# Optimization experiments

Measured on AMD Instinct MI355X. Metric: run time of the kernel, lower is better.

The kernel has to match this reference:

```python
import jax, jax.numpy as jnp
import numpy as np

N, E, H = 50000, 800000, 128

def _lin_params(key, out_dim, in_dim, bias=True, gain=1.0):
    k1, k2 = jax.random.split(key)
    lim = gain * np.sqrt(6.0 / (in_dim + out_dim))
    W = jax.random.uniform(k1, (out_dim, in_dim), jnp.float32, -lim, lim)
    b = jax.random.uniform(k2, (out_dim,), jnp.float32, -lim, lim) if bias else None
    return W, b

def setup_inputs() -> dict:
    key = jax.random.key(0)
    ks = jax.random.split(key, 12)
    h = jax.random.normal(ks[0], (N, H), jnp.float32)
    x = jax.random.normal(ks[1], (N, 3), jnp.float32)
    edge_index = jax.random.randint(ks[2], (2, E), 0, N, jnp.int64)
    We1, be1 = _lin_params(ks[3], H, 2 * H + 1)
    We2, be2 = _lin_params(ks[4], H, H)
    Wn1, bn1 = _lin_params(ks[5], H, 2 * H)
    Wn2, bn2 = _lin_params(ks[6], H, H)
    Wc1, bc1 = _lin_params(ks[7], H, H)
    Wc2, _ = _lin_params(ks[8], 1, H, bias=False, gain=0.001)
    gamma = jnp.ones((H,), jnp.float32)
    beta = jnp.zeros((H,), jnp.float32)
    return {"h": h, "x": x, "edge_index": edge_index,
            "We1": We1, "be1": be1, "We2": We2, "be2": be2,
            "Wn1": Wn1, "bn1": bn1, "Wn2": Wn2, "bn2": bn2,
            "Wc1": Wc1, "bc1": bc1, "Wc2": Wc2,
            "gamma": gamma, "beta": beta}

def _layer_norm(y, gamma, beta, eps=1e-5):
    mu = jnp.mean(y, axis=-1, keepdims=True)
    var = jnp.var(y, axis=-1, keepdims=True)
    return (y - mu) * jax.lax.rsqrt(var + eps) * gamma + beta

def reference(h, x, edge_index, We1, be1, We2, be2, Wn1, bn1, Wn2, bn2,
              Wc1, bc1, Wc2, gamma, beta):
    src, dst = edge_index[0], edge_index[1]
    diff = x[src] - x[dst]                                  # (E, 3)
    dist_sq = jnp.sum(diff * diff, axis=-1, keepdims=True)  # (E, 1)
    edge_in = jnp.concatenate([h[src], h[dst], dist_sq], axis=-1)  # (E, 2H+1)
    m = jax.nn.silu(edge_in @ We1.T + be1)
    m = jax.nn.silu(m @ We2.T + be2)                        # (E, H)
    num_nodes = h.shape[0]
    agg = jax.ops.segment_sum(m, dst, num_segments=num_nodes)            # (N, H)
    count = jax.ops.segment_sum(jnp.ones((dst.shape[0], 1), h.dtype), dst,
                                num_segments=num_nodes)
    count = jnp.maximum(count, 1.0)
    agg = agg / count
    u = jax.nn.silu(jnp.concatenate([h, agg], axis=-1) @ Wn1.T + bn1)
    h_out = h + (u @ Wn2.T + bn2)
    h_out = _layer_norm(h_out, gamma, beta)
    cw = jax.nn.silu(m @ Wc1.T + bc1) @ Wc2.T               # (E, 1)
    coord_agg = jax.ops.segment_sum(diff * cw, dst, num_segments=num_nodes) / count
    x_out = x + coord_agg
    return h_out, x_out
```

## Files before the change

kernel.cpp:

```cpp
#include <hip/hip_runtime.h>
#include <stdint.h>

using bf16x8 = __attribute__((ext_vector_type(8))) short;
using f32x4  = __attribute__((ext_vector_type(4))) float;

__device__ __forceinline__ unsigned short f2bf(float f) {
  uint32_t x = __float_as_uint(f);
  x += 0x7fffu + ((x >> 16) & 1u);
  return (unsigned short)(x >> 16);
}
__device__ __forceinline__ float bf2f(unsigned short u) {
  return __uint_as_float(((uint32_t)u) << 16);
}
__device__ __forceinline__ uint32_t cvtpk2(float lo, float hi) {
  uint32_t r;
  asm("v_cvt_pk_bf16_f32 %0, %1, %2" : "=v"(r) : "v"(lo), "v"(hi));
  return r;
}
__device__ __forceinline__ float silu_f(float v) {
  float e = __expf(-v);
  return v * __builtin_amdgcn_rcpf(1.0f + e);
}
__device__ __forceinline__ void unpack2(uint32_t u, float& lo, float& hi) {
  lo = __uint_as_float(u << 16);
  hi = __uint_as_float(u & 0xffff0000u);
}

__device__ __forceinline__ int msoff(int row, int col) {
  return row * 136 + ((((col >> 3) + row * 4) & 15) << 3) + (col & 7);
}
__device__ __forceinline__ int msoff_slot(int row, int slot) {
  return row * 136 + (((slot + row * 4) & 15) << 3);
}

__global__ void prep_kernel(const float* __restrict__ We1, const float* __restrict__ We2,
                            const float* __restrict__ Wn1, const float* __restrict__ Wn2,
                            const float* __restrict__ Wc1, const int* __restrict__ ei,
                            unsigned short* __restrict__ W1p, unsigned short* __restrict__ W2b,
                            unsigned short* __restrict__ N1b, unsigned short* __restrict__ N2b,
                            unsigned short* __restrict__ W3b, float* __restrict__ w1c,
                            int* __restrict__ flag) {
  int i = blockIdx.x * 256 + threadIdx.x;
  if (i < 256 * 128) {
    int c = i >> 7, k = i & 127;
    W1p[i] = f2bf(We1[(size_t)(c & 127) * 257 + ((c >> 7) << 7) + k]);
    N1b[i] = f2bf(Wn1[i]);
  }
  if (i < 128 * 128) {
    W2b[i] = f2bf(We2[i]);
    W3b[i] = f2bf(Wc1[i]);
    N2b[i] = f2bf(Wn2[i]);
  }
  if (i < 128) w1c[i] = We1[i * 257 + 256];
  if (i == 0) {
    int allz = 1;
    for (int k = 0; k < 64; ++k) allz &= (ei[2 * k + 1] == 0);
    *flag = allz;
  }
}

__global__ void hist_kernel(const int* __restrict__ ei, const int* __restrict__ flag,
                            int* __restrict__ deg, int E) {
  int e = blockIdx.x * 256 + threadIdx.x;
  if (e >= E) return;
  int d = (*flag) ? (int)((const long long*)ei)[(size_t)E + e] : ei[E + e];
  atomicAdd(&deg[d], 1);
}

__global__ void scanA_kernel(const int* __restrict__ deg, int* __restrict__ offs,
                             int* __restrict__ bsum, int N) {
  __shared__ int sh[256];
  int t = threadIdx.x, idx = blockIdx.x * 256 + t;
  int v = (idx < N) ? deg[idx] : 0;
  sh[t] = v;
  __syncthreads();
#pragma unroll
  for (int d = 1; d < 256; d <<= 1) {
    int u = (t >= d) ? sh[t - d] : 0;
    __syncthreads();
    sh[t] += u;
    __syncthreads();
  }
  if (idx < N) offs[idx] = sh[t] - v;
  if (t == 255) bsum[blockIdx.x] = sh[255];
}

__global__ void scanB_kernel(int* __restrict__ bsum, int* __restrict__ offs,
                             int nb, int N) {
  __shared__ int sh[256];
  int t = threadIdx.x;
  int v = (t < nb) ? bsum[t] : 0;
  sh[t] = v;
  __syncthreads();
#pragma unroll
  for (int d = 1; d < 256; d <<= 1) {
    int u = (t >= d) ? sh[t - d] : 0;
    __syncthreads();
    sh[t] += u;
    __syncthreads();
  }
  bsum[t] = sh[t] - v;
  if (t == 255) offs[N] = sh[255];
}

__global__ void scanC_kernel(const int* __restrict__ bsum, int* __restrict__ offs,
                             int* __restrict__ cursor, int N) {
  int idx = blockIdx.x * 256 + threadIdx.x;
  if (idx < N) {
    int o = offs[idx] + bsum[blockIdx.x];
    offs[idx] = o;
    cursor[idx] = o;
  }
}

__global__ void scatter_kernel(const int* __restrict__ ei, const int* __restrict__ flag,
                               int* __restrict__ cursor, int2* __restrict__ sd_s, int E) {
  int e = blockIdx.x * 256 + threadIdx.x;
  if (e >= E) return;
  int s, d;
  if (*flag) {
    s = (int)((const long long*)ei)[e];
    d = (int)((const long long*)ei)[(size_t)E + e];
  } else {
    s = ei[e];
    d = ei[E + e];
  }
  int pos = atomicAdd(&cursor[d], 1);
  int2 p; p.x = s; p.y = d;
  sd_s[pos] = p;
}

__global__ __launch_bounds__(256) void proj_kernel(
    const float* __restrict__ h, const float* __restrict__ be1,
    const unsigned short* __restrict__ W1p,
    unsigned short* __restrict__ Ps, unsigned short* __restrict__ Pd, int N) {
  const int tid = threadIdx.x;
  const int base = blockIdx.x * 64;
  const int w = tid >> 6, lane = tid & 63, lg = lane >> 4, lr = lane & 15;

  f32x4 acc[4][4];
#pragma unroll
  for (int m = 0; m < 4; ++m)
#pragma unroll
    for (int n = 0; n < 4; ++n) { f32x4 z = {0.f,0.f,0.f,0.f}; acc[m][n] = z; }

#pragma unroll
  for (int k0 = 0; k0 < 4; ++k0) {
    bf16x8 b[4];
#pragma unroll
    for (int n = 0; n < 4; ++n)
      b[n] = *(const bf16x8*)(W1p + ((w * 64 + n * 16 + lr) << 7) + k0 * 32 + lg * 8);
#pragma unroll
    for (int m = 0; m < 4; ++m) {
      int row = base + m * 16 + lr; if (row >= N) row = N - 1;
      const float* p = h + (size_t)row * 128 + k0 * 32 + lg * 8;
      float4 fa = *(const float4*)p;
      float4 fb = *(const float4*)(p + 4);
      uint32_t u0 = cvtpk2(fa.x, fa.y), u1 = cvtpk2(fa.z, fa.w);
      uint32_t u2 = cvtpk2(fb.x, fb.y), u3 = cvtpk2(fb.z, fb.w);
      union { uint32_t u[4]; bf16x8 v; } cv;
      cv.u[0] = u0; cv.u[1] = u1; cv.u[2] = u2; cv.u[3] = u3;
#pragma unroll
      for (int n = 0; n < 4; ++n)
        acc[m][n] = __builtin_amdgcn_mfma_f32_16x16x32_bf16(cv.v, b[n], acc[m][n], 0, 0, 0);
    }
  }
#pragma unroll
  for (int n = 0; n < 4; ++n) {
    int o = w * 64 + n * 16 + lr;
    unsigned short* dstp = (o < 128) ? Ps : Pd;
    int oo = o & 127;
    float add = (o < 128) ? be1[o] : 0.f;
#pragma unroll
    for (int m = 0; m < 4; ++m)
#pragma unroll
      for (int r = 0; r < 4; ++r) {
        int row = base + m * 16 + lg * 4 + r;
        if (row < N) dstp[(size_t)row * 128 + oo] = f2bf(acc[m][n][r] + add);
      }
  }
}

__global__ __launch_bounds__(256, 6) void edge_kernel(
    const unsigned short* __restrict__ Ps, const unsigned short* __restrict__ Pd,
    const float* __restrict__ x, const int2* __restrict__ sd_s,
    const float* __restrict__ w1c,
    const float* __restrict__ be2, const float* __restrict__ bc1,
    const float* __restrict__ Wc2,
    const unsigned short* __restrict__ W2b, const unsigned short* __restrict__ W3b,
    float* __restrict__ aggH, float* __restrict__ coordX, int E) {
  __shared__ __align__(16) unsigned short Ms[64 * 136];
  __shared__ float swred[4][64];
  __shared__ int   ssrc[64], sdst[64];
  __shared__ float sds[64];
  __shared__ float sdif[64][3];

  const int tid   = threadIdx.x;
  const int tbase = blockIdx.x * 64;
  const int w = tid >> 6, lane = tid & 63, lg = lane >> 4, lr = lane & 15;

  if (tid < 64) {
    int pos = tbase + tid;
    int s = 0, d = 0;
    if (pos < E) { int2 p = sd_s[pos]; s = p.x; d = p.y; }
    ssrc[tid] = s; sdst[tid] = d;
    float dx = x[s * 3 + 0] - x[d * 3 + 0];
    float dy = x[s * 3 + 1] - x[d * 3 + 1];
    float dz = x[s * 3 + 2] - x[d * 3 + 2];
    sdif[tid][0] = dx; sdif[tid][1] = dy; sdif[tid][2] = dz;
    sds[tid] = dx * dx + dy * dy + dz * dz;
  }
  __syncthreads();

  {
    const float4* w4 = (const float4*)w1c;
#pragma unroll
    for (int ch = 0; ch < 2; ++ch) {
      uint4 av[2], bv[2];
#pragma unroll
      for (int it = 0; it < 2; ++it) {
        int idx = tid + (ch * 2 + it) * 256;
        int e = idx >> 4, seg = idx & 15;
        av[it] = *(const uint4*)(Ps + (size_t)ssrc[e] * 128 + seg * 8);
        bv[it] = *(const uint4*)(Pd + (size_t)sdst[e] * 128 + seg * 8);
      }
#pragma unroll
      for (int it = 0; it < 2; ++it) {
        int idx = tid + (ch * 2 + it) * 256;
        int e = idx >> 4, seg = idx & 15;
        float dsv = sds[e];
        float4 wA = w4[seg * 2], wB = w4[seg * 2 + 1];
        float a0,a1,a2,a3,a4,a5,a6,a7, b0,b1,b2,b3,b4,b5,b6,b7;
        unpack2(((uint32_t*)&av[it])[0], a0, a1);
        unpack2(((uint32_t*)&av[it])[1], a2, a3);
        unpack2(((uint32_t*)&av[it])[2], a4, a5);
        unpack2(((uint32_t*)&av[it])[3], a6, a7);
        unpack2(((uint32_t*)&bv[it])[0], b0, b1);
        unpack2(((uint32_t*)&bv[it])[1], b2, b3);
        unpack2(((uint32_t*)&bv[it])[2], b4, b5);
        unpack2(((uint32_t*)&bv[it])[3], b6, b7);
        float v0 = silu_f(a0 + b0 + dsv * wA.x);
        float v1 = silu_f(a1 + b1 + dsv * wA.y);
        float v2 = silu_f(a2 + b2 + dsv * wA.z);
        float v3 = silu_f(a3 + b3 + dsv * wA.w);
        float v4 = silu_f(a4 + b4 + dsv * wB.x);
        float v5 = silu_f(a5 + b5 + dsv * wB.y);
        float v6 = silu_f(a6 + b6 + dsv * wB.z);
        float v7 = silu_f(a7 + b7 + dsv * wB.w);
        uint4 o;
        o.x = cvtpk2(v0, v1); o.y = cvtpk2(v2, v3);
        o.z = cvtpk2(v4, v5); o.w = cvtpk2(v6, v7);
        *(uint4*)(&Ms[msoff_slot(e, seg)]) = o;
      }
    }
  }
  __syncthreads();

  {
    f32x4 acc[4][2];
#pragma unroll
    for (int m = 0; m < 4; ++m) { f32x4 z = {0.f,0.f,0.f,0.f}; acc[m][0] = z; acc[m][1] = z; }
#pragma unroll
    for (int k0 = 0; k0 < 4; ++k0) {
      bf16x8 b0 = *(const bf16x8*)(W2b + ((w * 32 + lr)      << 7) + k0 * 32 + lg * 8);
      bf16x8 b1 = *(const bf16x8*)(W2b + ((w * 32 + 16 + lr) << 7) + k0 * 32 + lg * 8);
#pragma unroll
      for (int m = 0; m < 4; ++m) {
        int row = m * 16 + lr;
        bf16x8 a = *(const bf16x8*)(&Ms[msoff_slot(row, k0 * 4 + lg)]);
        acc[m][0] = __builtin_amdgcn_mfma_f32_16x16x32_bf16(a, b0, acc[m][0], 0, 0, 0);
        acc[m][1] = __builtin_amdgcn_mfma_f32_16x16x32_bf16(a, b1, acc[m][1], 0, 0, 0);
      }
    }
    uint32_t pk[4][2][2];
#pragma unroll
    for (int n = 0; n < 2; ++n) {
      int o = w * 32 + n * 16 + lr;
      float b2v = be2[o];
#pragma unroll
      for (int m = 0; m < 4; ++m)
#pragma unroll
        for (int r = 0; r < 4; r += 2)
          pk[m][n][r >> 1] = cvtpk2(silu_f(acc[m][n][r] + b2v),
                                    silu_f(acc[m][n][r + 1] + b2v));
    }
    __syncthreads();
#pragma unroll
    for (int n = 0; n < 2; ++n) {
      int o = w * 32 + n * 16 + lr;
#pragma unroll
      for (int m = 0; m < 4; ++m)
#pragma unroll
        for (int r = 0; r < 4; r += 2) {
          int row = m * 16 + lg * 4 + r;
          uint32_t u = pk[m][n][r >> 1];
          Ms[msoff(row, o)]     = (unsigned short)(u & 0xffffu);
          Ms[msoff(row + 1, o)] = (unsigned short)(u >> 16);
        }
    }
  }
  __syncthreads();

  {
    f32x4 acc[4][2];
#pragma unroll
    for (int m = 0; m < 4; ++m) { f32x4 z = {0.f,0.f,0.f,0.f}; acc[m][0] = z; acc[m][1] = z; }
#pragma unroll
    for (int k0 = 0; k0 < 4; ++k0) {
      bf16x8 b0 = *(const bf16x8*)(W3b + ((w * 32 + lr)      << 7) + k0 * 32 + lg * 8);
      bf16x8 b1 = *(const bf16x8*)(W3b + ((w * 32 + 16 + lr) << 7) + k0 * 32 + lg * 8);
#pragma unroll
      for (int m = 0; m < 4; ++m) {
        int row = m * 16 + lr;
        bf16x8 a = *(const bf16x8*)(&Ms[msoff_slot(row, k0 * 4 + lg)]);
        acc[m][0] = __builtin_amdgcn_mfma_f32_16x16x32_bf16(a, b0, acc[m][0], 0, 0, 0);
        acc[m][1] = __builtin_amdgcn_mfma_f32_16x16x32_bf16(a, b1, acc[m][1], 0, 0, 0);
      }
    }
    float pr[4][4];
#pragma unroll
    for (int m = 0; m < 4; ++m)
#pragma unroll
      for (int r = 0; r < 4; ++r) pr[m][r] = 0.f;
#pragma unroll
    for (int n = 0; n < 2; ++n) {
      int o = w * 32 + n * 16 + lr;
      float b3 = bc1[o], wc = Wc2[o];
#pragma unroll
      for (int m = 0; m < 4; ++m)
#pragma unroll
        for (int r = 0; r < 4; ++r)
          pr[m][r] += silu_f(acc[m][n][r] + b3) * wc;
    }
#pragma unroll
    for (int m = 0; m < 4; ++m)
#pragma unroll
      for (int r = 0; r < 4; ++r) {
        float v = pr[m][r];
        v += __shfl_xor(v, 1); v += __shfl_xor(v, 2);
        v += __shfl_xor(v, 4); v += __shfl_xor(v, 8);
        pr[m][r] = v;
      }
    if (lr == 0) {
#pragma unroll
      for (int m = 0; m < 4; ++m)
#pragma unroll
        for (int r = 0; r < 4; ++r)
          swred[w][m * 16 + lg * 4 + r] = pr[m][r];
    }
  }
  __syncthreads();

  const int nv = min(64, E - tbase);
  if (tid < 128) {
    int cp = tid & 63, hf = tid >> 6;
    int c0 = cp * 2;
    int e0 = hf * 32;
    int nvh = min(32, nv - e0);
    if (nvh > 0) {
      float r0 = 0.f, r1 = 0.f;
      int prev = sdst[e0];
#pragma unroll 4
      for (int j = 0; j < nvh; ++j) {
        int e = e0 + j;
        int d = sdst[e];
        uint32_t u = *(const uint32_t*)(&Ms[msoff(e, c0)]);
        if (d != prev) {
          atomicAdd(&aggH[(size_t)prev * 128 + c0],     r0);
          atomicAdd(&aggH[(size_t)prev * 128 + c0 + 1], r1);
          r0 = 0.f; r1 = 0.f; prev = d;
        }
        float lo, hi; unpack2(u, lo, hi);
        r0 += lo; r1 += hi;
      }
      atomicAdd(&aggH[(size_t)prev * 128 + c0],     r0);
      atomicAdd(&aggH[(size_t)prev * 128 + c0 + 1], r1);
    }
  } else if (tid >= 192 && tid < 198) {
    int t6 = tid - 192;
    int c3 = t6 % 3, hf = t6 / 3;
    int e0 = hf * 32;
    int nvh = min(32, nv - e0);
    if (nvh > 0) {
      float run = 0.f;
      int prev = sdst[e0];
#pragma unroll 4
      for (int j = 0; j < nvh; ++j) {
        int e = e0 + j;
        int d = sdst[e];
        float cwv = swred[0][e] + swred[1][e] + swred[2][e] + swred[3][e];
        if (d != prev) {
          atomicAdd(&coordX[(size_t)prev * 3 + c3], run);
          run = 0.f; prev = d;
        }
        run += sdif[e][c3] * cwv;
      }
      atomicAdd(&coordX[(size_t)prev * 3 + c3], run);
    }
  }
}

__global__ __launch_bounds__(256) void node_kernel(
    const float* __restrict__ h, const float* __restrict__ x,
    const float* __restrict__ bn1, const float* __restrict__ bn2,
    const float* __restrict__ gamma, const float* __restrict__ beta,
    const unsigned short* __restrict__ N1b, const unsigned short* __restrict__ N2b,
    float* __restrict__ aggH, float* __restrict__ coordX,
    const int* __restrict__ deg, int N) {
  __shared__ __align__(16) unsigned short In[64][264];
  __shared__ __align__(16) unsigned short U[64][136];
  __shared__ float scnt[64];

  const int tid  = threadIdx.x;
  const int base = blockIdx.x * 64;
  const int w    = tid >> 6;
  const int lane = tid & 63;
  const int lg   = lane >> 4, lr = lane & 15;
  const int w16  = w * 16;

  if (tid < 64) {
    int n = base + tid;
    scnt[tid] = (n < N) ? fmaxf((float)deg[n], 1.0f) : 1.0f;
  }
  __syncthreads();

#pragma unroll
  for (int it = 0; it < 8; ++it) {
    int idx = tid + it * 256;
    int i = idx >> 5, seg = idx & 31;
    int n = base + i; if (n >= N) n = N - 1;
    float sc = 1.0f;
    const float* p;
    if (seg < 16) { p = h + (size_t)n * 128 + seg * 8; }
    else          { p = aggH + (size_t)n * 128 + (seg - 16) * 8; sc = 1.0f / scnt[i]; }
    float4 a = *(const float4*)p;
    float4 b = *(const float4*)(p + 4);
    uint32_t u0 = cvtpk2(a.x * sc, a.y * sc);
    uint32_t u1 = cvtpk2(a.z * sc, a.w * sc);
    uint32_t u2 = cvtpk2(b.x * sc, b.y * sc);
    uint32_t u3 = cvtpk2(b.z * sc, b.w * sc);
    uint4 v = {u0, u1, u2, u3};
    *(uint4*)&In[i][seg * 8] = v;
  }
  __syncthreads();

  {
    f32x4 acc[8];
#pragma unroll
    for (int n = 0; n < 8; ++n) { f32x4 z = {0.f,0.f,0.f,0.f}; acc[n] = z; }
#pragma unroll
    for (int k0 = 0; k0 < 8; ++k0) {
      bf16x8 a = *(const bf16x8*)(&In[w16 + lr][k0 * 32 + lg * 8]);
#pragma unroll
      for (int n = 0; n < 8; ++n) {
        bf16x8 b = *(const bf16x8*)(N1b + ((n * 16 + lr) << 8) + k0 * 32 + lg * 8);
        acc[n] = __builtin_amdgcn_mfma_f32_16x16x32_bf16(a, b, acc[n], 0, 0, 0);
      }
    }
#pragma unroll
    for (int n = 0; n < 8; ++n) {
      int o = n * 16 + lr;
      float b1 = bn1[o];
#pragma unroll
      for (int r = 0; r < 4; ++r) {
        int me = lg * 4 + r;
        U[w16 + me][o] = f2bf(silu_f(acc[n][r] + b1));
      }
    }
  }

  float* hp = (float*)&In[0][0];
  {
    f32x4 acc[8];
#pragma unroll
    for (int n = 0; n < 8; ++n) { f32x4 z = {0.f,0.f,0.f,0.f}; acc[n] = z; }
#pragma unroll
    for (int k0 = 0; k0 < 4; ++k0) {
      bf16x8 a = *(const bf16x8*)(&U[w16 + lr][k0 * 32 + lg * 8]);
#pragma unroll
      for (int n = 0; n < 8; ++n) {
        bf16x8 b = *(const bf16x8*)(N2b + ((n * 16 + lr) << 7) + k0 * 32 + lg * 8);
        acc[n] = __builtin_amdgcn_mfma_f32_16x16x32_bf16(a, b, acc[n], 0, 0, 0);
      }
    }
#pragma unroll
    for (int n = 0; n < 8; ++n) {
      int o = n * 16 + lr;
      float b2 = bn2[o];
#pragma unroll
      for (int r = 0; r < 4; ++r) {
        int me = w16 + lg * 4 + r;
        int ng = base + me; if (ng >= N) ng = N - 1;
        hp[(size_t)me * 132 + o] = acc[n][r] + b2 + h[(size_t)ng * 128 + o];
      }
    }
  }
  __syncthreads();

  {
    int r = tid >> 2, q = tid & 3;
    int ng = base + r;
    float s = 0.f, s2 = 0.f;
#pragma unroll
    for (int j = 0; j < 32; ++j) {
      float v = hp[(size_t)r * 132 + j * 4 + q];
      s += v; s2 += v * v;
    }
    s  += __shfl_xor(s, 1);  s  += __shfl_xor(s, 2);
    s2 += __shfl_xor(s2, 1); s2 += __shfl_xor(s2, 2);
    float mu  = s * (1.0f / 128.0f);
    float var = s2 * (1.0f / 128.0f) - mu * mu;
    float rs  = rsqrtf(var + 1e-5f);
    if (ng < N) {
#pragma unroll
      for (int j = 0; j < 32; ++j) {
        int o = j * 4 + q;
        float v = (hp[(size_t)r * 132 + o] - mu) * rs * gamma[o] + beta[o];
        aggH[(size_t)ng * 128 + o] = v;
      }
    }
  }

  if (tid < 192) {
    int i = tid / 3, c = tid % 3;
    int n2 = base + i;
    if (n2 < N) {
      size_t off = (size_t)n2 * 3 + c;
      coordX[off] = x[off] + coordX[off] / scnt[i];
    }
  }
}

extern "C" void kernel_launch(void* const* d_in, const int* in_sizes, int n_in,
                              void* d_out, int out_size, void* d_ws, size_t ws_size,
                              hipStream_t stream) {
  const float* h    = (const float*)d_in[0];
  const float* x    = (const float*)d_in[1];
  const int*   ei   = (const int*)d_in[2];
  const float* We1  = (const float*)d_in[3];
  const float* be1  = (const float*)d_in[4];
  const float* We2  = (const float*)d_in[5];
  const float* be2  = (const float*)d_in[6];
  const float* Wn1  = (const float*)d_in[7];
  const float* bn1  = (const float*)d_in[8];
  const float* Wn2  = (const float*)d_in[9];
  const float* bn2  = (const float*)d_in[10];
  const float* Wc1  = (const float*)d_in[11];
  const float* bc1  = (const float*)d_in[12];
  const float* Wc2  = (const float*)d_in[13];
  const float* gamma = (const float*)d_in[14];
  const float* beta  = (const float*)d_in[15];

  int N = in_sizes[0] / 128;
  int E = in_sizes[2] / 2;

  float* aggH   = (float*)d_out;
  float* coordX = (float*)d_out + (size_t)N * 128;

  char* ws = (char*)d_ws;
  size_t off = 0;
  auto alloc = [&](size_t bytes) {
    char* p = ws + off;
    off = (off + bytes + 255) & ~(size_t)255;
    return p;
  };
  unsigned short* Ps     = (unsigned short*)alloc((size_t)N * 128 * 2);
  unsigned short* Pd     = (unsigned short*)alloc((size_t)N * 128 * 2);
  unsigned short* W1p    = (unsigned short*)alloc(256 * 128 * 2);
  unsigned short* W2b    = (unsigned short*)alloc(128 * 128 * 2);
  unsigned short* N1b    = (unsigned short*)alloc(128 * 256 * 2);
  unsigned short* N2b    = (unsigned short*)alloc(128 * 128 * 2);
  unsigned short* W3b    = (unsigned short*)alloc(128 * 128 * 2);
  float*          w1c    = (float*)alloc(128 * 4);
  int*            flag   = (int*)alloc(4);
  int*            deg    = (int*)alloc((size_t)N * 4);
  int*            offs   = (int*)alloc(((size_t)N + 1) * 4);
  int*            cursor = (int*)alloc((size_t)N * 4);
  int*            bsum   = (int*)alloc(256 * 4);
  int2*           sd_s   = (int2*)alloc((size_t)E * 8);
  (void)ws_size;

  int nb = (N + 255) / 256;

  hipMemsetAsync(d_out, 0, (size_t)out_size * 4, stream);
  hipMemsetAsync(deg, 0, (size_t)N * 4, stream);

  prep_kernel<<<128, 256, 0, stream>>>(We1, We2, Wn1, Wn2, Wc1, ei,
                                       W1p, W2b, N1b, N2b, W3b, w1c, flag);
  hist_kernel<<<(E + 255) / 256, 256, 0, stream>>>(ei, flag, deg, E);
  scanA_kernel<<<nb, 256, 0, stream>>>(deg, offs, bsum, N);
  scanB_kernel<<<1, 256, 0, stream>>>(bsum, offs, nb, N);
  scanC_kernel<<<nb, 256, 0, stream>>>(bsum, offs, cursor, N);
  scatter_kernel<<<(E + 255) / 256, 256, 0, stream>>>(ei, flag, cursor, sd_s, E);
  proj_kernel<<<(N + 63) / 64, 256, 0, stream>>>(h, be1, W1p, Ps, Pd, N);
  edge_kernel<<<(E + 63) / 64, 256, 0, stream>>>(Ps, Pd, x, sd_s, w1c,
                                                 be2, bc1, Wc2, W2b, W3b,
                                                 aggH, coordX, E);
  node_kernel<<<(N + 63) / 64, 256, 0, stream>>>(h, x, bn1, bn2, gamma, beta, N1b, N2b,
                                                 aggH, coordX, deg, N);
}
```

Before: 379.3 us.

## Remap edge blocks per XCD, widen scatter threads, and stream node inputs directly

The edge kernel now remaps block IDs so consecutive logical edge tiles land on the same XCD, which keeps L2 locality for the sorted-by-destination atomics. The scatter phase now uses all 256 threads, each covering 16 edges instead of 32, and the coordinate scatter uses 12 threads. The node kernel drops the staging LDS buffer and loads h/agg rows straight from global memory into MFMA A operands, sharing one buffer for U and hp. This cuts shared memory to raise occupancy, at the cost of more atomics and repeated global loads across k0.

After: 393.6 us. +3.8%, slower.

```diff
diff --git a/kernel.cpp b/kernel.cpp
--- a/kernel.cpp
+++ b/kernel.cpp
@@ -196,13 +196,17 @@
   __shared__ float sdif[64][3];
 
   const int tid   = threadIdx.x;
-  const int tbase = blockIdx.x * 64;
+  const int nwg = gridDim.x;
+  const int q = nwg >> 3, r = nwg & 7;
+  const int xcd = blockIdx.x & 7, pos = blockIdx.x >> 3;
+  const int logical = (xcd < r ? xcd * (q + 1) : r * (q + 1) + (xcd - r) * q) + pos;
+  const int tbase = logical * 64;
   const int w = tid >> 6, lane = tid & 63, lg = lane >> 4, lr = lane & 15;
 
   if (tid < 64) {
-    int pos = tbase + tid;
+    int p0 = tbase + tid;
     int s = 0, d = 0;
-    if (pos < E) { int2 p = sd_s[pos]; s = p.x; d = p.y; }
+    if (p0 < E) { int2 p = sd_s[p0]; s = p.x; d = p.y; }
     ssrc[tid] = s; sdst[tid] = d;
     float dx = x[s * 3 + 0] - x[d * 3 + 0];
     float dy = x[s * 3 + 1] - x[d * 3 + 1];
@@ -280,9 +284,9 @@
 #pragma unroll
       for (int m = 0; m < 4; ++m)
 #pragma unroll
-        for (int r = 0; r < 4; r += 2)
-          pk[m][n][r >> 1] = cvtpk2(silu_f(acc[m][n][r] + b2v),
-                                    silu_f(acc[m][n][r + 1] + b2v));
+        for (int r2 = 0; r2 < 4; r2 += 2)
+          pk[m][n][r2 >> 1] = cvtpk2(silu_f(acc[m][n][r2] + b2v),
+                                     silu_f(acc[m][n][r2 + 1] + b2v));
     }
     __syncthreads();
 #pragma unroll
@@ -291,9 +295,9 @@
 #pragma unroll
       for (int m = 0; m < 4; ++m)
 #pragma unroll
-        for (int r = 0; r < 4; r += 2) {
-          int row = m * 16 + lg * 4 + r;
-          uint32_t u = pk[m][n][r >> 1];
+        for (int r2 = 0; r2 < 4; r2 += 2) {
+          int row = m * 16 + lg * 4 + r2;
+          uint32_t u = pk[m][n][r2 >> 1];
           Ms[msoff(row, o)]     = (unsigned short)(u & 0xffffu);
           Ms[msoff(row + 1, o)] = (unsigned short)(u >> 16);
         }
@@ -321,7 +325,7 @@
 #pragma unroll
     for (int m = 0; m < 4; ++m)
 #pragma unroll
-      for (int r = 0; r < 4; ++r) pr[m][r] = 0.f;
+      for (int r2 = 0; r2 < 4; ++r2) pr[m][r2] = 0.f;
 #pragma unroll
     for (int n = 0; n < 2; ++n) {
       int o = w * 32 + n * 16 + lr;
@@ -329,34 +333,34 @@
 #pragma unroll
       for (int m = 0; m < 4; ++m)
 #pragma unroll
-        for (int r = 0; r < 4; ++r)
-          pr[m][r] += silu_f(acc[m][n][r] + b3) * wc;
+        for (int r2 = 0; r2 < 4; ++r2)
+          pr[m][r2] += silu_f(acc[m][n][r2] + b3) * wc;
     }
 #pragma unroll
     for (int m = 0; m < 4; ++m)
 #pragma unroll
-      for (int r = 0; r < 4; ++r) {
-        float v = pr[m][r];
+      for (int r2 = 0; r2 < 4; ++r2) {
+        float v = pr[m][r2];
         v += __shfl_xor(v, 1); v += __shfl_xor(v, 2);
         v += __shfl_xor(v, 4); v += __shfl_xor(v, 8);
-        pr[m][r] = v;
+        pr[m][r2] = v;
       }
     if (lr == 0) {
 #pragma unroll
       for (int m = 0; m < 4; ++m)
 #pragma unroll
-        for (int r = 0; r < 4; ++r)
-          swred[w][m * 16 + lg * 4 + r] = pr[m][r];
+        for (int r2 = 0; r2 < 4; ++r2)
+          swred[w][m * 16 + lg * 4 + r2] = pr[m][r2];
     }
   }
   __syncthreads();
 
   const int nv = min(64, E - tbase);
-  if (tid < 128) {
-    int cp = tid & 63, hf = tid >> 6;
+  {
+    int cp = tid & 63, qt = tid >> 6;
     int c0 = cp * 2;
-    int e0 = hf * 32;
-    int nvh = min(32, nv - e0);
+    int e0 = qt * 16;
+    int nvh = min(16, nv - e0);
     if (nvh > 0) {
       float r0 = 0.f, r1 = 0.f;
       int prev = sdst[e0];
@@ -376,11 +380,11 @@
       atomicAdd(&aggH[(size_t)prev * 128 + c0],     r0);
       atomicAdd(&aggH[(size_t)prev * 128 + c0 + 1], r1);
     }
-  } else if (tid >= 192 && tid < 198) {
-    int t6 = tid - 192;
-    int c3 = t6 % 3, hf = t6 / 3;
-    int e0 = hf * 32;
-    int nvh = min(32, nv - e0);
+  }
+  if (tid < 12) {
+    int c3 = tid % 3, qt = tid / 3;
+    int e0 = qt * 16;
+    int nvh = min(16, nv - e0);
     if (nvh > 0) {
       float run = 0.f;
       int prev = sdst[e0];
@@ -407,9 +411,9 @@
     const unsigned short* __restrict__ N1b, const unsigned short* __restrict__ N2b,
     float* __restrict__ aggH, float* __restrict__ coordX,
     const int* __restrict__ deg, int N) {
-  __shared__ __align__(16) unsigned short In[64][264];
-  __shared__ __align__(16) unsigned short U[64][136];
+  __shared__ __align__(16) float hp[64 * 132];
   __shared__ float scnt[64];
+  unsigned short* U = (unsigned short*)hp;
 
   const int tid  = threadIdx.x;
   const int base = blockIdx.x * 64;
@@ -424,25 +428,8 @@
   }
   __syncthreads();
 
-#pragma unroll
-  for (int it = 0; it < 8; ++it) {
-    int idx = tid + it * 256;
-    int i = idx >> 5, seg = idx & 31;
-    int n = base + i; if (n >= N) n = N - 1;
-    float sc = 1.0f;
-    const float* p;
-    if (seg < 16) { p = h + (size_t)n * 128 + seg * 8; }
-    else          { p = aggH + (size_t)n * 128 + (seg - 16) * 8; sc = 1.0f / scnt[i]; }
-    float4 a = *(const float4*)p;
-    float4 b = *(const float4*)(p + 4);
-    uint32_t u0 = cvtpk2(a.x * sc, a.y * sc);
-    uint32_t u1 = cvtpk2(a.z * sc, a.w * sc);
-    uint32_t u2 = cvtpk2(b.x * sc, b.y * sc);
-    uint32_t u3 = cvtpk2(b.z * sc, b.w * sc);
-    uint4 v = {u0, u1, u2, u3};
-    *(uint4*)&In[i][seg * 8] = v;
-  }
-  __syncthreads();
+  int arow = base + w16 + lr; if (arow >= N) arow = N - 1;
+  const float sc = 1.0f / scnt[w16 + lr];
 
   {
     f32x4 acc[8];
@@ -450,11 +437,20 @@
     for (int n = 0; n < 8; ++n) { f32x4 z = {0.f,0.f,0.f,0.f}; acc[n] = z; }
 #pragma unroll
     for (int k0 = 0; k0 < 8; ++k0) {
-      bf16x8 a = *(const bf16x8*)(&In[w16 + lr][k0 * 32 + lg * 8]);
+      const float* p = (k0 < 4) ? (h    + (size_t)arow * 128 + k0 * 32 + lg * 8)
+                                : (aggH + (size_t)arow * 128 + (k0 - 4) * 32 + lg * 8);
+      float s = (k0 < 4) ? 1.0f : sc;
+      float4 fa = *(const float4*)p;
+      float4 fb = *(const float4*)(p + 4);
+      union { uint32_t u[4]; bf16x8 v; } cv;
+      cv.u[0] = cvtpk2(fa.x * s, fa.y * s);
+      cv.u[1] = cvtpk2(fa.z * s, fa.w * s);
+      cv.u[2] = cvtpk2(fb.x * s, fb.y * s);
+      cv.u[3] = cvtpk2(fb.z * s, fb.w * s);
 #pragma unroll
       for (int n = 0; n < 8; ++n) {
         bf16x8 b = *(const bf16x8*)(N1b + ((n * 16 + lr) << 8) + k0 * 32 + lg * 8);
-        acc[n] = __builtin_amdgcn_mfma_f32_16x16x32_bf16(a, b, acc[n], 0, 0, 0);
+        acc[n] = __builtin_amdgcn_mfma_f32_16x16x32_bf16(cv.v, b, acc[n], 0, 0, 0);
       }
     }
 #pragma unroll
@@ -464,25 +460,25 @@
 #pragma unroll
       for (int r = 0; r < 4; ++r) {
         int me = lg * 4 + r;
-        U[w16 + me][o] = f2bf(silu_f(acc[n][r] + b1));
-      }
-    }
-  }
-
-  float* hp = (float*)&In[0][0];
+        U[(size_t)(w16 + me) * 136 + o] = f2bf(silu_f(acc[n][r] + b1));
+      }
+    }
+  }
+
   {
     f32x4 acc[8];
 #pragma unroll
     for (int n = 0; n < 8; ++n) { f32x4 z = {0.f,0.f,0.f,0.f}; acc[n] = z; }
 #pragma unroll
     for (int k0 = 0; k0 < 4; ++k0) {
-      bf16x8 a = *(const bf16x8*)(&U[w16 + lr][k0 * 32 + lg * 8]);
+      bf16x8 a = *(const bf16x8*)(&U[(size_t)(w16 + lr) * 136 + k0 * 32 + lg * 8]);
 #pragma unroll
       for (int n = 0; n < 8; ++n) {
         bf16x8 b = *(const bf16x8*)(N2b + ((n * 16 + lr) << 7) + k0 * 32 + lg * 8);
         acc[n] = __builtin_amdgcn_mfma_f32_16x16x32_bf16(a, b, acc[n], 0, 0, 0);
       }
     }
+    __syncthreads();
 #pragma unroll
     for (int n = 0; n < 8; ++n) {
       int o = n * 16 + lr;
@@ -498,12 +494,12 @@
   __syncthreads();
 
   {
-    int r = tid >> 2, q = tid & 3;
+    int r = tid >> 2, qq = tid & 3;
     int ng = base + r;
     float s = 0.f, s2 = 0.f;
 #pragma unroll
     for (int j = 0; j < 32; ++j) {
-      float v = hp[(size_t)r * 132 + j * 4 + q];
+      float v = hp[(size_t)r * 132 + j * 4 + qq];
       s += v; s2 += v * v;
     }
     s  += __shfl_xor(s, 1);  s  += __shfl_xor(s, 2);
@@ -514,7 +510,7 @@
     if (ng < N) {
 #pragma unroll
       for (int j = 0; j < 32; ++j) {
-        int o = j * 4 + q;
+        int o = j * 4 + qq;
         float v = (hp[(size_t)r * 132 + o] - mu) * rs * gamma[o] + beta[o];
         aggH[(size_t)ng * 128 + o] = v;
       }
```

## Replace atomics with plain stores for segments fully owned by one block

Applied to the files above, without the earlier changes.

The edge kernel now reads the CSR offsets to mark, per edge, whether it starts or ends a destination segment. When a thread's run of edges covers a whole destination segment, it writes aggH and coordX with plain stores instead of atomicAdd. The hist and scatter kernels also process two edges per thread. This removes most global atomics in the segment reduction, at the cost of extra offs loads and relying on the output being zeroed beforehand.

Result: no change. 381.7 us (+0.6%).

```diff
diff --git a/kernel.cpp b/kernel.cpp
--- a/kernel.cpp
+++ b/kernel.cpp
@@ -61,10 +61,19 @@
 
 __global__ void hist_kernel(const int* __restrict__ ei, const int* __restrict__ flag,
                             int* __restrict__ deg, int E) {
-  int e = blockIdx.x * 256 + threadIdx.x;
-  if (e >= E) return;
-  int d = (*flag) ? (int)((const long long*)ei)[(size_t)E + e] : ei[E + e];
-  atomicAdd(&deg[d], 1);
+  int e0 = (blockIdx.x * 256 + threadIdx.x) * 2;
+  if (e0 >= E) return;
+  bool has1 = (e0 + 1 < E);
+  int d0, d1 = 0;
+  if (*flag) {
+    const long long* p = (const long long*)ei + E + e0;
+    d0 = (int)p[0]; if (has1) d1 = (int)p[1];
+  } else {
+    const int* p = ei + E + e0;
+    d0 = p[0]; if (has1) d1 = p[1];
+  }
+  atomicAdd(&deg[d0], 1);
+  if (has1) atomicAdd(&deg[d1], 1);
 }
 
 __global__ void scanA_kernel(const int* __restrict__ deg, int* __restrict__ offs,
@@ -115,19 +124,24 @@
 
 __global__ void scatter_kernel(const int* __restrict__ ei, const int* __restrict__ flag,
                                int* __restrict__ cursor, int2* __restrict__ sd_s, int E) {
-  int e = blockIdx.x * 256 + threadIdx.x;
-  if (e >= E) return;
-  int s, d;
+  int e0 = (blockIdx.x * 256 + threadIdx.x) * 2;
+  if (e0 >= E) return;
+  int ne = min(2, E - e0);
+  int ss[2], dd[2];
   if (*flag) {
-    s = (int)((const long long*)ei)[e];
-    d = (int)((const long long*)ei)[(size_t)E + e];
+    const long long* ps = (const long long*)ei + e0;
+    const long long* pd = (const long long*)ei + E + e0;
+    for (int j = 0; j < ne; ++j) { ss[j] = (int)ps[j]; dd[j] = (int)pd[j]; }
   } else {
-    s = ei[e];
-    d = ei[E + e];
-  }
-  int pos = atomicAdd(&cursor[d], 1);
-  int2 p; p.x = s; p.y = d;
-  sd_s[pos] = p;
+    const int* ps = ei + e0;
+    const int* pd = ei + E + e0;
+    for (int j = 0; j < ne; ++j) { ss[j] = ps[j]; dd[j] = pd[j]; }
+  }
+  for (int j = 0; j < ne; ++j) {
+    int pos = atomicAdd(&cursor[dd[j]], 1);
+    int2 p; p.x = ss[j]; p.y = dd[j];
+    sd_s[pos] = p;
+  }
 }
 
 __global__ __launch_bounds__(256) void proj_kernel(
@@ -156,10 +170,9 @@
       const float* p = h + (size_t)row * 128 + k0 * 32 + lg * 8;
       float4 fa = *(const float4*)p;
       float4 fb = *(const float4*)(p + 4);
-      uint32_t u0 = cvtpk2(fa.x, fa.y), u1 = cvtpk2(fa.z, fa.w);
-      uint32_t u2 = cvtpk2(fb.x, fb.y), u3 = cvtpk2(fb.z, fb.w);
       union { uint32_t u[4]; bf16x8 v; } cv;
-      cv.u[0] = u0; cv.u[1] = u1; cv.u[2] = u2; cv.u[3] = u3;
+      cv.u[0] = cvtpk2(fa.x, fa.y); cv.u[1] = cvtpk2(fa.z, fa.w);
+      cv.u[2] = cvtpk2(fb.x, fb.y); cv.u[3] = cvtpk2(fb.z, fb.w);
 #pragma unroll
       for (int n = 0; n < 4; ++n)
         acc[m][n] = __builtin_amdgcn_mfma_f32_16x16x32_bf16(cv.v, b[n], acc[m][n], 0, 0, 0);
@@ -184,6 +197,7 @@
 __global__ __launch_bounds__(256, 6) void edge_kernel(
     const unsigned short* __restrict__ Ps, const unsigned short* __restrict__ Pd,
     const float* __restrict__ x, const int2* __restrict__ sd_s,
+    const int* __restrict__ offs,
     const float* __restrict__ w1c,
     const float* __restrict__ be2, const float* __restrict__ bc1,
     const float* __restrict__ Wc2,
@@ -194,16 +208,23 @@
   __shared__ int   ssrc[64], sdst[64];
   __shared__ float sds[64];
   __shared__ float sdif[64][3];
+  __shared__ unsigned char sA[64], sB[64];
 
   const int tid   = threadIdx.x;
   const int tbase = blockIdx.x * 64;
   const int w = tid >> 6, lane = tid & 63, lg = lane >> 4, lr = lane & 15;
 
   if (tid < 64) {
-    int pos = tbase + tid;
+    int p0 = tbase + tid;
     int s = 0, d = 0;
-    if (pos < E) { int2 p = sd_s[pos]; s = p.x; d = p.y; }
+    unsigned char fa = 0, fb = 0;
+    if (p0 < E) {
+      int2 p = sd_s[p0]; s = p.x; d = p.y;
+      fa = (offs[d] == p0);
+      fb = (offs[d + 1] == p0 + 1);
+    }
     ssrc[tid] = s; sdst[tid] = d;
+    sA[tid] = fa; sB[tid] = fb;
     float dx = x[s * 3 + 0] - x[d * 3 + 0];
     float dy = x[s * 3 + 1] - x[d * 3 + 1];
     float dz = x[s * 3 + 2] - x[d * 3 + 2];
@@ -280,9 +301,9 @@
 #pragma unroll
       for (int m = 0; m < 4; ++m)
 #pragma unroll
-        for (int r = 0; r < 4; r += 2)
-          pk[m][n][r >> 1] = cvtpk2(silu_f(acc[m][n][r] + b2v),
-                                    silu_f(acc[m][n][r + 1] + b2v));
+        for (int r2 = 0; r2 < 4; r2 += 2)
+          pk[m][n][r2 >> 1] = cvtpk2(silu_f(acc[m][n][r2] + b2v),
+                                     silu_f(acc[m][n][r2 + 1] + b2v));
     }
     __syncthreads();
 #pragma unroll
@@ -291,9 +312,9 @@
 #pragma unroll
       for (int m = 0; m < 4; ++m)
 #pragma unroll
-        for (int r = 0; r < 4; r += 2) {
-          int row = m * 16 + lg * 4 + r;
-          uint32_t u = pk[m][n][r >> 1];
+        for (int r2 = 0; r2 < 4; r2 += 2) {
+          int row = m * 16 + lg * 4 + r2;
+          uint32_t u = pk[m][n][r2 >> 1];
           Ms[msoff(row, o)]     = (unsigned short)(u & 0xffffu);
           Ms[msoff(row + 1, o)] = (unsigned short)(u >> 16);
         }
@@ -321,7 +342,7 @@
 #pragma unroll
     for (int m = 0; m < 4; ++m)
 #pragma unroll
-      for (int r = 0; r < 4; ++r) pr[m][r] = 0.f;
+      for (int r2 = 0; r2 < 4; ++r2) pr[m][r2] = 0.f;
 #pragma unroll
     for (int n = 0; n < 2; ++n) {
       int o = w * 32 + n * 16 + lr;
@@ -329,24 +350,24 @@
 #pragma unroll
       for (int m = 0; m < 4; ++m)
 #pragma unroll
-        for (int r = 0; r < 4; ++r)
-          pr[m][r] += silu_f(acc[m][n][r] + b3) * wc;
+        for (int r2 = 0; r2 < 4; ++r2)
+          pr[m][r2] += silu_f(acc[m][n][r2] + b3) * wc;
     }
 #pragma unroll
     for (int m = 0; m < 4; ++m)
 #pragma unroll
-      for (int r = 0; r < 4; ++r) {
-        float v = pr[m][r];
+      for (int r2 = 0; r2 < 4; ++r2) {
+        float v = pr[m][r2];
         v += __shfl_xor(v, 1); v += __shfl_xor(v, 2);
         v += __shfl_xor(v, 4); v += __shfl_xor(v, 8);
-        pr[m][r] = v;
+        pr[m][r2] = v;
       }
     if (lr == 0) {
 #pragma unroll
       for (int m = 0; m < 4; ++m)
 #pragma unroll
-        for (int r = 0; r < 4; ++r)
-          swred[w][m * 16 + lg * 4 + r] = pr[m][r];
+        for (int r2 = 0; r2 < 4; ++r2)
+          swred[w][m * 16 + lg * 4 + r2] = pr[m][r2];
     }
   }
   __syncthreads();
@@ -360,21 +381,24 @@
     if (nvh > 0) {
       float r0 = 0.f, r1 = 0.f;
       int prev = sdst[e0];
+      int es = e0;
 #pragma unroll 4
       for (int j = 0; j < nvh; ++j) {
         int e = e0 + j;
         int d = sdst[e];
         uint32_t u = *(const uint32_t*)(&Ms[msoff(e, c0)]);
         if (d != prev) {
-          atomicAdd(&aggH[(size_t)prev * 128 + c0],     r0);
-          atomicAdd(&aggH[(size_t)prev * 128 + c0 + 1], r1);
-          r0 = 0.f; r1 = 0.f; prev = d;
+          float* a0 = &aggH[(size_t)prev * 128 + c0];
+          if (sA[es] && sB[e - 1]) { a0[0] = r0; a0[1] = r1; }
+          else { atomicAdd(a0, r0); atomicAdd(a0 + 1, r1); }
+          r0 = 0.f; r1 = 0.f; prev = d; es = e;
         }
         float lo, hi; unpack2(u, lo, hi);
         r0 += lo; r1 += hi;
       }
-      atomicAdd(&aggH[(size_t)prev * 128 + c0],     r0);
-      atomicAdd(&aggH[(size_t)prev * 128 + c0 + 1], r1);
+      float* a0 = &aggH[(size_t)prev * 128 + c0];
+      if (sA[es] && sB[e0 + nvh - 1]) { a0[0] = r0; a0[1] = r1; }
+      else { atomicAdd(a0, r0); atomicAdd(a0 + 1, r1); }
     }
   } else if (tid >= 192 && tid < 198) {
     int t6 = tid - 192;
@@ -384,18 +408,21 @@
     if (nvh > 0) {
       float run = 0.f;
       int prev = sdst[e0];
+      int es = e0;
 #pragma unroll 4
       for (int j = 0; j < nvh; ++j) {
         int e = e0 + j;
         int d = sdst[e];
         float cwv = swred[0][e] + swred[1][e] + swred[2][e] + swred[3][e];
         if (d != prev) {
-          atomicAdd(&coordX[(size_t)prev * 3 + c3], run);
-          run = 0.f; prev = d;
+          if (sA[es] && sB[e - 1]) coordX[(size_t)prev * 3 + c3] = run;
+          else atomicAdd(&coordX[(size_t)prev * 3 + c3], run);
+          run = 0.f; prev = d; es = e;
         }
         run += sdif[e][c3] * cwv;
       }
-      atomicAdd(&coordX[(size_t)prev * 3 + c3], run);
+      if (sA[es] && sB[e0 + nvh - 1]) coordX[(size_t)prev * 3 + c3] = run;
+      else atomicAdd(&coordX[(size_t)prev * 3 + c3], run);
     }
   }
 }
@@ -581,19 +608,20 @@
   (void)ws_size;
 
   int nb = (N + 255) / 256;
+  int epairs = (E + 1) / 2;
 
   hipMemsetAsync(d_out, 0, (size_t)out_size * 4, stream);
   hipMemsetAsync(deg, 0, (size_t)N * 4, stream);
 
   prep_kernel<<<128, 256, 0, stream>>>(We1, We2, Wn1, Wn2, Wc1, ei,
                                        W1p, W2b, N1b, N2b, W3b, w1c, flag);
-  hist_kernel<<<(E + 255) / 256, 256, 0, stream>>>(ei, flag, deg, E);
+  hist_kernel<<<(epairs + 255) / 256, 256, 0, stream>>>(ei, flag, deg, E);
   scanA_kernel<<<nb, 256, 0, stream>>>(deg, offs, bsum, N);
   scanB_kernel<<<1, 256, 0, stream>>>(bsum, offs, nb, N);
   scanC_kernel<<<nb, 256, 0, stream>>>(bsum, offs, cursor, N);
-  scatter_kernel<<<(E + 255) / 256, 256, 0, stream>>>(ei, flag, cursor, sd_s, E);
+  scatter_kernel<<<(epairs + 255) / 256, 256, 0, stream>>>(ei, flag, cursor, sd_s, E);
   proj_kernel<<<(N + 63) / 64, 256, 0, stream>>>(h, be1, W1p, Ps, Pd, N);
-  edge_kernel<<<(E + 63) / 64, 256, 0, stream>>>(Ps, Pd, x, sd_s, w1c,
+  edge_kernel<<<(E + 63) / 64, 256, 0, stream>>>(Ps, Pd, x, sd_s, offs, w1c,
                                                  be2, bc1, Wc2, W2b, W3b,
                                                  aggH, coordX, E);
   node_kernel<<<(N + 63) / 64, 256, 0, stream>>>(h, x, bn1, bn2, gamma, beta, N1b, N2b,
```
